# Optimization experiments

Hardware: AMD Instinct MI355X
Metric: run time of the kernel (lower is better)

## Reference

```python
import jax, jax.numpy as jnp
import numpy as np

WH, WW = 7, 7
NUM_HEADS = 8

def _relative_position_index(Wh, Ww):
    coords = np.stack(np.meshgrid(np.arange(Wh), np.arange(Ww), indexing='ij'))  # (2, Wh, Ww)
    cf = coords.reshape(2, -1)                       # (2, N)
    rc = cf[:, :, None] - cf[:, None, :]             # (2, N, N)
    rc = rc.transpose(1, 2, 0).astype(np.int64)      # (N, N, 2)
    rc[..., 0] += Wh - 1
    rc[..., 1] += Ww - 1
    rc[..., 0] *= 2 * Ww - 1
    return rc.sum(-1)                                # (N, N)

_REL_IDX = jnp.asarray(_relative_position_index(WH, WW))


def setup_inputs() -> dict:
    key = jax.random.key(0)
    ks = jax.random.split(key, 9)
    B_, N, C = 2048, 49, 256
    nW = 64
    return {
        'x': jax.random.normal(ks[0], (B_, N, C), jnp.float32),
        'mask': jax.random.normal(ks[1], (nW, N, N), jnp.float32),
        'sal_fg_attn_mask': jax.random.normal(ks[2], (B_, N, N), jnp.float32),
        'sal_bg_attn_mask': jax.random.normal(ks[3], (B_, N, N), jnp.float32),
        'qkv_w': jax.random.normal(ks[4], (3 * C, C), jnp.float32) * 0.02,
        'qkv_b': jax.random.normal(ks[5], (3 * C,), jnp.float32) * 0.02,
        'proj_w': jax.random.normal(ks[6], (C, C), jnp.float32) * 0.02,
        'proj_b': jax.random.normal(ks[7], (C,), jnp.float32) * 0.02,
        'rel_pos_bias_table': jax.random.normal(ks[8], ((2 * WH - 1) * (2 * WW - 1), NUM_HEADS), jnp.float32) * 0.02,
    }


def reference(x, mask, sal_fg_attn_mask, sal_bg_attn_mask, qkv_w, qkv_b, proj_w, proj_b, rel_pos_bias_table):
    B_, N, C = x.shape
    H = NUM_HEADS
    hd = C // H
    scale = hd ** -0.5

    qkv = x @ qkv_w.T + qkv_b                        # (B_, N, 3C)
    qkv = qkv.reshape(B_, N, 3, H, hd).transpose(2, 0, 3, 1, 4)  # (3, B_, H, N, hd)
    q, k, v = qkv[0] * scale, qkv[1], qkv[2]

    attn = jnp.einsum('bhqd,bhkd->bhqk', q, k)       # (B_, H, N, N)
    bias = rel_pos_bias_table[_REL_IDX]              # (N, N, H)
    attn = attn + bias.transpose(2, 0, 1)[None]      # broadcast over B_

    attn_fg = attn + sal_fg_attn_mask[:, None]
    attn_bg = attn + sal_bg_attn_mask[:, None]

    nW = mask.shape[0]
    m = mask[None, :, None]                          # (1, nW, 1, N, N)

    def masked_softmax(a):
        a = a.reshape(B_ // nW, nW, H, N, N) + m
        return jax.nn.softmax(a.reshape(B_, H, N, N), axis=-1)

    attn = masked_softmax(attn)
    attn_fg = masked_softmax(attn_fg)
    attn_bg = masked_softmax(attn_bg)

    def av(a):
        return jnp.einsum('bhqk,bhkd->bqhd', a, v).reshape(B_, N, C)

    out = av(attn) + av(attn_fg) - av(attn_bg)
    return out @ proj_w.T + proj_b
```

## Files before the change

### kernel.cpp

```cpp
#include <hip/hip_runtime.h>
#include <hip/hip_bf16.h>
#include <math.h>


#define B_TOT   2048
#define NTOK    49
#define CDIM    256
#define NHEAD   8
#define HDIM    32
#define MROWS   (B_TOT * NTOK)
#define QKV_N   (3 * CDIM)
#define NCHUNK  8
#define B_CH    (B_TOT / NCHUNK)
#define MR_CH   (B_CH * NTOK)

#define LOG2E 1.4426950408889634f

#if __has_builtin(__builtin_amdgcn_exp2f)
#define EXP2(x) __builtin_amdgcn_exp2f(x)
#else
#define EXP2(x) __expf((x) * 0.6931471805599453f)
#endif

typedef __attribute__((ext_vector_type(8))) short short8;
typedef __attribute__((ext_vector_type(4))) float floatx4;

typedef unsigned int u32_g __attribute__((address_space(1)));
typedef unsigned int u32_l __attribute__((address_space(3)));

__device__ __forceinline__ void gld_lds16(const void* g, void* l) {
    __builtin_amdgcn_global_load_lds((const u32_g*)g, (u32_l*)l, 16, 0, 0);
}

__device__ __forceinline__ void cast8(const float* __restrict__ in,
                                      __hip_bfloat16* __restrict__ out, int i) {
    const float4* p = (const float4*)in + (size_t)i * 2;
    float4 a = p[0], b = p[1];
    __hip_bfloat16 r[8];
    r[0] = __float2bfloat16(a.x); r[1] = __float2bfloat16(a.y);
    r[2] = __float2bfloat16(a.z); r[3] = __float2bfloat16(a.w);
    r[4] = __float2bfloat16(b.x); r[5] = __float2bfloat16(b.y);
    r[6] = __float2bfloat16(b.z); r[7] = __float2bfloat16(b.w);
    *(uint4*)(out + (size_t)i * 8) = *(const uint4*)r;
}

__device__ __forceinline__ void exp4(const float* __restrict__ in,
                                     float* __restrict__ out, int i) {
    float4 a = ((const float4*)in)[i];
    float4 r;
    r.x = EXP2(a.x * LOG2E); r.y = EXP2(a.y * LOG2E);
    r.z = EXP2(a.z * LOG2E); r.w = EXP2(a.w * LOG2E);
    ((float4*)out)[i] = r;
}

__global__ __launch_bounds__(256) void pre_masks(
    const float* __restrict__ qkv_w,
    const float* __restrict__ proj_w,
    const float* __restrict__ wmask,
    const float* __restrict__ table,
    const float* __restrict__ fg,
    const float* __restrict__ bg,
    __hip_bfloat16* __restrict__ qwb,
    __hip_bfloat16* __restrict__ pwb,
    float* __restrict__ wmp,
    float* __restrict__ Fgp,
    float* __restrict__ Bgp)
{
    const int bid = blockIdx.x;
    const int t = threadIdx.x;
    if (bid < 96) {
        cast8(qkv_w, qwb, bid * 256 + t);
    } else if (bid < 128) {
        cast8(proj_w, pwb, (bid - 96) * 256 + t);
    } else if (bid < 8320) {
        const int idx = (bid - 128) * 256 + t;
        const int col = idx & 63, row = (idx >> 6) & 63;
        const int h = (idx >> 12) & 7, win = idx >> 15;
        float v = -1e30f;
        if (row < 49 && col < 49) {
            const int qi = row / 7, qj = row % 7;
            const int ki = col / 7, kj = col % 7;
            const int ti = (qi - ki + 6) * 13 + (qj - kj + 6);
            v = (wmask[win * 2401 + row * 49 + col] + table[ti * 8 + h]) * LOG2E;
        }
        wmp[idx] = v;
    } else if (bid < 13122) {
        exp4(fg, Fgp, (bid - 8320) * 256 + t);
    } else {
        exp4(bg, Bgp, (bid - 13122) * 256 + t);
    }
}

__global__ __launch_bounds__(256) void cast_x(
    const float* __restrict__ in, __hip_bfloat16* __restrict__ out)
{
    cast8(in, out, blockIdx.x * 256 + threadIdx.x);
}

template<int NDIM, bool OUT_BF16>
__global__ __launch_bounds__(256) void gemm_mfma(
    const __hip_bfloat16* __restrict__ A,
    const __hip_bfloat16* __restrict__ W,
    const float* __restrict__ bias,
    void* __restrict__ Yv)
{
    const int K = 256;
    __shared__ short As[128 * 64];
    __shared__ short Bs[128 * 64];
    const int t = threadIdx.x;
    const int lane = t & 63, w = t >> 6;
    const int wr = w >> 1, wc = w & 1;
    const int q = lane >> 4, l15 = lane & 15;

    constexpr int NBX = NDIM / 128;
    const int nwg = NBX * (int)gridDim.y;
    const int orig = (int)blockIdx.y * NBX + (int)blockIdx.x;
    const int xcd = orig & 7, rest = orig >> 3;
    const int qq = nwg >> 3, rr = nwg & 7;
    const int bid = (xcd < rr ? xcd * (qq + 1) : rr * (qq + 1) + (xcd - rr) * qq) + rest;
    const int m0 = (bid / NBX) * 128, n0 = (bid % NBX) * 128;

    const int srow = t >> 3, skb = t & 7;
    const int gkb = skb ^ (srow & 7);
    const __hip_bfloat16* Ag = A + (size_t)(m0 + srow) * K + gkb * 8;
    const __hip_bfloat16* Wg = W + (size_t)(n0 + srow) * K + gkb * 8;

    floatx4 acc[4][4] = {};
    const int swz = l15 & 7;

    for (int k0 = 0; k0 < K; k0 += 64) {
        __syncthreads();
        #pragma unroll
        for (int i = 0; i < 4; i++) {
            gld_lds16(Ag + (size_t)(i * 32) * K + k0, &As[i * 2048 + w * 512]);
            gld_lds16(Wg + (size_t)(i * 32) * K + k0, &Bs[i * 2048 + w * 512]);
        }
        __syncthreads();
        #pragma unroll
        for (int kk = 0; kk < 2; kk++) {
            const int kbs = ((kk << 2) + q) ^ swz;
            short8 af[4], bf[4];
            #pragma unroll
            for (int i = 0; i < 4; i++) {
                af[i] = *(const short8*)&As[(wr * 64 + i * 16 + l15) * 64 + kbs * 8];
                bf[i] = *(const short8*)&Bs[(wc * 64 + i * 16 + l15) * 64 + kbs * 8];
            }
            #pragma unroll
            for (int i = 0; i < 4; i++)
                #pragma unroll
                for (int j = 0; j < 4; j++)
                    acc[i][j] = __builtin_amdgcn_mfma_f32_16x16x32_bf16(
                        af[i], bf[j], acc[i][j], 0, 0, 0);
        }
    }

    #pragma unroll
    for (int j = 0; j < 4; j++) {
        const int n = n0 + wc * 64 + j * 16 + l15;
        const float bv = bias[n];
        #pragma unroll
        for (int i = 0; i < 4; i++) {
            #pragma unroll
            for (int r = 0; r < 4; r++) {
                const int m = m0 + wr * 64 + i * 16 + q * 4 + r;
                const float val = acc[i][j][r] + bv;
                if (OUT_BF16)
                    ((__hip_bfloat16*)Yv)[(size_t)m * NDIM + n] = __float2bfloat16(val);
                else
                    ((float*)Yv)[(size_t)m * NDIM + n] = val;
            }
        }
    }
}

__global__ __launch_bounds__(256, 6) void attn_kernel(
    const __hip_bfloat16* __restrict__ Y,
    const float* __restrict__ wmp,
    const float* __restrict__ Fgp,
    const float* __restrict__ Bgp,
    __hip_bfloat16* __restrict__ O,
    int b_base)
{
    __shared__ __hip_bfloat16 sQ[64 * 40];
    __shared__ __hip_bfloat16 sK[64 * 40];
    __shared__ __hip_bfloat16 sVt[32 * 72];
    __shared__ __hip_bfloat16 sP[64 * 72];

    const int blk = blockIdx.x;
    const int b = b_base + (blk >> 6) * 8 + (blk & 7);
    const int h = (blk >> 3) & 7;
    const int t = threadIdx.x;
    const int w = t >> 6, lane = t & 63;
    const int quad = lane >> 4, l15 = lane & 15;
    const float SC = 0.17677669529663687f * LOG2E;

    const float* wmb = wmp + (((size_t)(b & 63) * 8 + h) << 12);
    const float* fgb = Fgp + (size_t)b * (NTOK * NTOK);
    const float* bgb = Bgp + (size_t)b * (NTOK * NTOK);
    float mwm[16], mfg[16], mbg[16];
    #pragma unroll
    for (int r = 0; r < 4; r++) {
        const int row = w * 16 + quad * 4 + r;
        const int rc49 = min(row, 48) * 49;
        const float* pw = wmb + row * 64 + l15;
        const float* pf = fgb + rc49 + l15;
        const float* pb = bgb + rc49 + l15;
        mwm[r * 4 + 0] = pw[0];  mwm[r * 4 + 1] = pw[16];
        mwm[r * 4 + 2] = pw[32]; mwm[r * 4 + 3] = pw[48];
        mfg[r * 4 + 0] = pf[0];  mfg[r * 4 + 1] = pf[16];
        mfg[r * 4 + 2] = pf[32]; mfg[r * 4 + 3] = fgb[rc49 + 48];
        mbg[r * 4 + 0] = pb[0];  mbg[r * 4 + 1] = pb[16];
        mbg[r * 4 + 2] = pb[32]; mbg[r * 4 + 3] = bgb[rc49 + 48];
    }
    const __hip_bfloat16* Yb = Y + (size_t)b * NTOK * QKV_N + h * HDIM;
    if (t < 196) {
        const int n = t >> 2, c = t & 3;
        uint4 qv = *(const uint4*)(Yb + (size_t)n * QKV_N + c * 8);
        uint4 kv = *(const uint4*)(Yb + (size_t)n * QKV_N + 256 + c * 8);
        uint4 vv = *(const uint4*)(Yb + (size_t)n * QKV_N + 512 + c * 8);
        *(uint4*)(sQ + n * 40 + c * 8) = qv;
        *(uint4*)(sK + n * 40 + c * 8) = kv;
        const __hip_bfloat16* vp = (const __hip_bfloat16*)&vv;
        #pragma unroll
        for (int j = 0; j < 8; j++)
            sVt[(c * 8 + j) * 72 + n] = vp[j];
    }
    {
        unsigned int* pK = (unsigned int*)sK;
        #pragma unroll
        for (int i = 980 + t; i < 1280; i += 256) pK[i] = 0u;
    }
    {
        const __hip_bfloat16 z = __float2bfloat16(0.f);
        #pragma unroll
        for (int it = 0; it < 2; it++) {
            const int idx = t + it * 256;
            const int d = idx >> 4, c = 49 + (idx & 15);
            sVt[d * 72 + c] = z;
        }
    }
    __syncthreads();

    floatx4 acc[4];
    {
        short8 af = *(const short8*)(sQ + (w * 16 + l15) * 40 + quad * 8);
        #pragma unroll
        for (int nt = 0; nt < 4; nt++) {
            short8 bf = *(const short8*)(sK + (nt * 16 + l15) * 40 + quad * 8);
            floatx4 z = {};
            acc[nt] = __builtin_amdgcn_mfma_f32_16x16x32_bf16(af, bf, z, 0, 0, 0);
        }
    }

    float e0[16];
    #pragma unroll
    for (int r = 0; r < 4; r++)
        #pragma unroll
        for (int nt = 0; nt < 4; nt++)
            e0[r * 4 + nt] = EXP2(fmaf(acc[nt][r], SC, mwm[r * 4 + nt]));
    #pragma unroll
    for (int i = 0; i < 16; i++) mfg[i] *= e0[i];
    #pragma unroll
    for (int i = 0; i < 16; i++) mbg[i] *= e0[i];

    float s0[4], sf[4], sb[4];
    #pragma unroll
    for (int r = 0; r < 4; r++) {
        s0[r] = (e0[r * 4] + e0[r * 4 + 1]) + (e0[r * 4 + 2] + e0[r * 4 + 3]);
        sf[r] = (mfg[r * 4] + mfg[r * 4 + 1]) + (mfg[r * 4 + 2] + mfg[r * 4 + 3]);
        sb[r] = (mbg[r * 4] + mbg[r * 4 + 1]) + (mbg[r * 4 + 2] + mbg[r * 4 + 3]);
    }
    #pragma unroll
    for (int st = 1; st < 16; st <<= 1)
        #pragma unroll
        for (int r = 0; r < 4; r++) {
            s0[r] += __shfl_xor(s0[r], st);
            sf[r] += __shfl_xor(sf[r], st);
            sb[r] += __shfl_xor(sb[r], st);
        }

    float pc[16];
    #pragma unroll
    for (int r = 0; r < 4; r++) {
        const float r0 = __builtin_amdgcn_rcpf(s0[r]);
        const float rf = __builtin_amdgcn_rcpf(sf[r]);
        const float rb = -__builtin_amdgcn_rcpf(sb[r]);
        #pragma unroll
        for (int nt = 0; nt < 4; nt++) {
            const int i = r * 4 + nt;
            pc[i] = fmaf(mbg[i], rb, fmaf(mfg[i], rf, e0[i] * r0));
        }
    }

    #pragma unroll
    for (int r = 0; r < 4; r++) {
        const int row = w * 16 + quad * 4 + r;
        #pragma unroll
        for (int nt = 0; nt < 4; nt++)
            sP[row * 72 + nt * 16 + l15] = __float2bfloat16(pc[r * 4 + nt]);
    }
    __syncthreads();

    floatx4 o0 = {}, o1 = {};
    {
        short8 a0  = *(const short8*)(sP + (w * 16 + l15) * 72 + quad * 8);
        short8 a1  = *(const short8*)(sP + (w * 16 + l15) * 72 + 32 + quad * 8);
        short8 b00 = *(const short8*)(sVt + l15 * 72 + quad * 8);
        short8 b01 = *(const short8*)(sVt + l15 * 72 + 32 + quad * 8);
        short8 b10 = *(const short8*)(sVt + (16 + l15) * 72 + quad * 8);
        short8 b11 = *(const short8*)(sVt + (16 + l15) * 72 + 32 + quad * 8);
        o0 = __builtin_amdgcn_mfma_f32_16x16x32_bf16(a0, b00, o0, 0, 0, 0);
        o0 = __builtin_amdgcn_mfma_f32_16x16x32_bf16(a1, b01, o0, 0, 0, 0);
        o1 = __builtin_amdgcn_mfma_f32_16x16x32_bf16(a0, b10, o1, 0, 0, 0);
        o1 = __builtin_amdgcn_mfma_f32_16x16x32_bf16(a1, b11, o1, 0, 0, 0);
    }
    __hip_bfloat16* Ob = O + (size_t)b * NTOK * CDIM + h * HDIM;
    #pragma unroll
    for (int r = 0; r < 4; r++) {
        const int m = w * 16 + quad * 4 + r;
        if (m < NTOK) {
            Ob[(size_t)m * CDIM + l15]      = __float2bfloat16(o0[r]);
            Ob[(size_t)m * CDIM + 16 + l15] = __float2bfloat16(o1[r]);
        }
    }
}

extern "C" void kernel_launch(void* const* d_in, const int* in_sizes, int n_in,
                              void* d_out, int out_size, void* d_ws, size_t ws_size,
                              hipStream_t stream) {
    const float* x      = (const float*)d_in[0];
    const float* mask   = (const float*)d_in[1];
    const float* fg     = (const float*)d_in[2];
    const float* bg     = (const float*)d_in[3];
    const float* qkv_w  = (const float*)d_in[4];
    const float* qkv_b  = (const float*)d_in[5];
    const float* proj_w = (const float*)d_in[6];
    const float* proj_b = (const float*)d_in[7];
    const float* table  = (const float*)d_in[8];
    float* out = (float*)d_out;

    char* ws = (char*)d_ws;
    __hip_bfloat16* xb  = (__hip_bfloat16*)(ws);
    __hip_bfloat16* Ybf = (__hip_bfloat16*)(ws + 51380224);
    float* wmp = (float*)(ws + 205520896);
    float* Fgp = (float*)(ws + 213909504);
    float* Bgp = (float*)(ws + 233578496);
    __hip_bfloat16* qwb = (__hip_bfloat16*)(ws + 256901120);
    __hip_bfloat16* pwb = (__hip_bfloat16*)(ws + 257294336);
    __hip_bfloat16* Obf = xb;

    dim3 blk(256);
    pre_masks<<<dim3(17924), blk, 0, stream>>>(
        qkv_w, proj_w, mask, table, fg, bg, qwb, pwb, wmp, Fgp, Bgp);

    for (int c = 0; c < NCHUNK; c++) {
        const size_t ro = (size_t)c * MR_CH;
        const float* xc = x + ro * CDIM;
        __hip_bfloat16* xbc = xb + ro * CDIM;
        __hip_bfloat16* Yc  = Ybf + ro * QKV_N;
        __hip_bfloat16* Oc  = Obf + ro * CDIM;
        float* outc = out + ro * CDIM;

        cast_x<<<dim3(MR_CH * CDIM / 8 / 256), blk, 0, stream>>>(xc, xbc);
        gemm_mfma<QKV_N, true><<<dim3(QKV_N / 128, MR_CH / 128), blk, 0, stream>>>(
            xbc, qwb, qkv_b, Yc);
        attn_kernel<<<dim3(B_CH * NHEAD), blk, 0, stream>>>(
            Ybf, wmp, Fgp, Bgp, Obf, c * B_CH);
        gemm_mfma<CDIM, false><<<dim3(CDIM / 128, MR_CH / 128), blk, 0, stream>>>(
            Oc, pwb, proj_b, outc);
    }
}
```

Measured before the change: 484.5 us.

## Fuse QKV projection into attention kernel and drop chunked launches

Each attention block now loads its window of x in fp32, converts it to bf16 into swizzled shared memory, and computes its head's Q, K and V slices with MFMA before running attention. This removes the separate cast kernel, the QKV GEMM and the global bf16 QKV intermediate, and replaces the 8-chunk launch loop with one full-batch launch. The cost is that x is re-read once per head, shared memory grows and the occupancy hint drops from 6 to 3 blocks.

```diff
diff --git a/kernel.cpp b/kernel.cpp
--- a/kernel.cpp
+++ b/kernel.cpp
@@ -10,9 +10,6 @@
 #define HDIM    32
 #define MROWS   (B_TOT * NTOK)
 #define QKV_N   (3 * CDIM)
-#define NCHUNK  8
-#define B_CH    (B_TOT / NCHUNK)
-#define MR_CH   (B_CH * NTOK)
 
 #define LOG2E 1.4426950408889634f
 
@@ -91,12 +88,6 @@
     }
 }
 
-__global__ __launch_bounds__(256) void cast_x(
-    const float* __restrict__ in, __hip_bfloat16* __restrict__ out)
-{
-    cast8(in, out, blockIdx.x * 256 + threadIdx.x);
-}
-
 template<int NDIM, bool OUT_BF16>
 __global__ __launch_bounds__(256) void gemm_mfma(
     const __hip_bfloat16* __restrict__ A,
@@ -173,21 +164,23 @@
     }
 }
 
-__global__ __launch_bounds__(256, 6) void attn_kernel(
-    const __hip_bfloat16* __restrict__ Y,
+__global__ __launch_bounds__(256, 3) void fused_attn(
+    const float* __restrict__ x,
+    const __hip_bfloat16* __restrict__ Wq,
+    const float* __restrict__ qkv_b,
     const float* __restrict__ wmp,
     const float* __restrict__ Fgp,
     const float* __restrict__ Bgp,
-    __hip_bfloat16* __restrict__ O,
-    int b_base)
+    __hip_bfloat16* __restrict__ O)
 {
+    __shared__ __hip_bfloat16 sX[64 * 256];
     __shared__ __hip_bfloat16 sQ[64 * 40];
     __shared__ __hip_bfloat16 sK[64 * 40];
     __shared__ __hip_bfloat16 sVt[32 * 72];
-    __shared__ __hip_bfloat16 sP[64 * 72];
+    __hip_bfloat16* sP = sX;
 
     const int blk = blockIdx.x;
-    const int b = b_base + (blk >> 6) * 8 + (blk & 7);
+    const int b = (blk >> 6) * 8 + (blk & 7);
     const int h = (blk >> 3) & 7;
     const int t = threadIdx.x;
     const int w = t >> 6, lane = t & 63;
@@ -212,31 +205,60 @@
         mbg[r * 4 + 0] = pb[0];  mbg[r * 4 + 1] = pb[16];
         mbg[r * 4 + 2] = pb[32]; mbg[r * 4 + 3] = bgb[rc49 + 48];
     }
-    const __hip_bfloat16* Yb = Y + (size_t)b * NTOK * QKV_N + h * HDIM;
-    if (t < 196) {
-        const int n = t >> 2, c = t & 3;
-        uint4 qv = *(const uint4*)(Yb + (size_t)n * QKV_N + c * 8);
-        uint4 kv = *(const uint4*)(Yb + (size_t)n * QKV_N + 256 + c * 8);
-        uint4 vv = *(const uint4*)(Yb + (size_t)n * QKV_N + 512 + c * 8);
-        *(uint4*)(sQ + n * 40 + c * 8) = qv;
-        *(uint4*)(sK + n * 40 + c * 8) = kv;
-        const __hip_bfloat16* vp = (const __hip_bfloat16*)&vv;
-        #pragma unroll
-        for (int j = 0; j < 8; j++)
-            sVt[(c * 8 + j) * 72 + n] = vp[j];
-    }
-    {
-        unsigned int* pK = (unsigned int*)sK;
-        #pragma unroll
-        for (int i = 980 + t; i < 1280; i += 256) pK[i] = 0u;
-    }
-    {
-        const __hip_bfloat16 z = __float2bfloat16(0.f);
-        #pragma unroll
-        for (int it = 0; it < 2; it++) {
-            const int idx = t + it * 256;
-            const int d = idx >> 4, c = 49 + (idx & 15);
-            sVt[d * 72 + c] = z;
+
+    const float* xb_ = x + (size_t)b * NTOK * CDIM;
+    #pragma unroll
+    for (int it = 0; it < 16; it++) {
+        const int i = t + it * 256;
+        const int row = i >> 6, c = i & 63;
+        const float4 v4 = *(const float4*)(xb_ + (size_t)min(row, 48) * CDIM + c * 4);
+        __hip_bfloat16 hv[4];
+        hv[0] = __float2bfloat16(v4.x); hv[1] = __float2bfloat16(v4.y);
+        hv[2] = __float2bfloat16(v4.z); hv[3] = __float2bfloat16(v4.w);
+        *(uint2*)&sX[row * 256 + (((c >> 1) ^ (row & 7)) << 3) + (c & 1) * 4] =
+            *(const uint2*)hv;
+    }
+    __syncthreads();
+
+    const int ntw = (w < 2) ? 2 : 1;
+    const int wbase = (w == 0) ? h * HDIM
+                    : (w == 1) ? CDIM + h * HDIM
+                               : 2 * CDIM + h * HDIM + ((w == 3) ? 16 : 0);
+    floatx4 qa[4][2] = {};
+    #pragma unroll
+    for (int s = 0; s < 8; s++) {
+        short8 axf[4];
+        #pragma unroll
+        for (int i = 0; i < 4; i++)
+            axf[i] = *(const short8*)&sX[(i * 16 + l15) * 256 +
+                                         ((((s << 2) | quad) ^ (l15 & 7)) << 3)];
+        #pragma unroll
+        for (int jt = 0; jt < 2; jt++) {
+            if (jt < ntw) {
+                short8 wf = *(const short8*)&Wq[(size_t)(wbase + jt * 16 + l15) * CDIM
+                                                + s * 32 + quad * 8];
+                #pragma unroll
+                for (int i = 0; i < 4; i++)
+                    qa[i][jt] = __builtin_amdgcn_mfma_f32_16x16x32_bf16(
+                        axf[i], wf, qa[i][jt], 0, 0, 0);
+            }
+        }
+    }
+    #pragma unroll
+    for (int jt = 0; jt < 2; jt++) {
+        if (jt < ntw) {
+            const float bv = qkv_b[wbase + jt * 16 + l15];
+            #pragma unroll
+            for (int i = 0; i < 4; i++) {
+                #pragma unroll
+                for (int r = 0; r < 4; r++) {
+                    const int m = i * 16 + quad * 4 + r;
+                    const __hip_bfloat16 hv = __float2bfloat16(qa[i][jt][r] + bv);
+                    if (w == 0)      sQ[m * 40 + jt * 16 + l15] = hv;
+                    else if (w == 1) sK[m * 40 + jt * 16 + l15] = hv;
+                    else             sVt[((w == 2) ? l15 : 16 + l15) * 72 + m] = hv;
+                }
+            }
         }
     }
     __syncthreads();
@@ -340,33 +362,18 @@
     float* out = (float*)d_out;
 
     char* ws = (char*)d_ws;
-    __hip_bfloat16* xb  = (__hip_bfloat16*)(ws);
-    __hip_bfloat16* Ybf = (__hip_bfloat16*)(ws + 51380224);
+    __hip_bfloat16* Obf = (__hip_bfloat16*)(ws);
     float* wmp = (float*)(ws + 205520896);
     float* Fgp = (float*)(ws + 213909504);
     float* Bgp = (float*)(ws + 233578496);
     __hip_bfloat16* qwb = (__hip_bfloat16*)(ws + 256901120);
     __hip_bfloat16* pwb = (__hip_bfloat16*)(ws + 257294336);
-    __hip_bfloat16* Obf = xb;
 
     dim3 blk(256);
     pre_masks<<<dim3(17924), blk, 0, stream>>>(
         qkv_w, proj_w, mask, table, fg, bg, qwb, pwb, wmp, Fgp, Bgp);
-
-    for (int c = 0; c < NCHUNK; c++) {
-        const size_t ro = (size_t)c * MR_CH;
-        const float* xc = x + ro * CDIM;
-        __hip_bfloat16* xbc = xb + ro * CDIM;
-        __hip_bfloat16* Yc  = Ybf + ro * QKV_N;
-        __hip_bfloat16* Oc  = Obf + ro * CDIM;
-        float* outc = out + ro * CDIM;
-
-        cast_x<<<dim3(MR_CH * CDIM / 8 / 256), blk, 0, stream>>>(xc, xbc);
-        gemm_mfma<QKV_N, true><<<dim3(QKV_N / 128, MR_CH / 128), blk, 0, stream>>>(
-            xbc, qwb, qkv_b, Yc);
-        attn_kernel<<<dim3(B_CH * NHEAD), blk, 0, stream>>>(
-            Ybf, wmp, Fgp, Bgp, Obf, c * B_CH);
-        gemm_mfma<CDIM, false><<<dim3(CDIM / 128, MR_CH / 128), blk, 0, stream>>>(
-            Oc, pwb, proj_b, outc);
-    }
-}
+    fused_attn<<<dim3(B_TOT * NHEAD), blk, 0, stream>>>(
+        x, qwb, qkv_b, wmp, Fgp, Bgp, Obf);
+    gemm_mfma<CDIM, false><<<dim3(CDIM / 128, MROWS / 128), blk, 0, stream>>>(
+        Obf, pwb, proj_b, out);
+}
```

Result: slower. 495.3 us (+2.2%).
